# Kernel tuning notes

Hardware: AMD Instinct MI355X
Metric: run time of the kernel (lower is better)

## Reference

```python
import jax, jax.numpy as jnp
import numpy as np

IN_F = 4096
OUT_F = 4096
RANK = 16
ALPHA = 16
SCALING = ALPHA / RANK  # 1.0


def setup_inputs() -> dict:
    key = jax.random.key(0)
    k_x, k_w, k_b, k_a = jax.random.split(key, 4)
    x = jax.random.normal(k_x, (4, 2048, IN_F), dtype=jnp.float32)
    # frozen base linear params
    W = jax.random.normal(k_w, (OUT_F, IN_F), dtype=jnp.float32) * (1.0 / np.sqrt(IN_F))
    b = jax.random.normal(k_b, (OUT_F,), dtype=jnp.float32) * 0.01
    # LoRA params: A kaiming-uniform-like, B zeros per initial_weights(); use small
    bound = np.sqrt(6.0 / IN_F)  # kaiming_uniform(a=sqrt(5)) bound approx
    lora_A = jax.random.uniform(k_a, (RANK, IN_F), dtype=jnp.float32, minval=-bound, maxval=bound)
    lora_B = jax.random.normal(jax.random.fold_in(key, 7), (OUT_F, RANK), dtype=jnp.float32) * 0.01
    lora_bias = jnp.zeros((OUT_F,), dtype=jnp.float32)
    return {"x": x, "W": W, "b": b, "lora_A": lora_A, "lora_B": lora_B, "lora_bias": lora_bias}


def reference(x, W, b, lora_A, lora_B, lora_bias):
    # Original: F.linear(x, W + scaling*B@A, bias=b + lora_bias); dropout is Identity (p=0).
    # Algebraically equivalent form avoiding the [out,in] delta materialization:
    # y = x@W^T + scaling * (x@A^T)@B^T + (b + lora_bias)
    base = jnp.einsum('bsi,oi->bso', x, W)
    low = jnp.einsum('bsr,or->bso', jnp.einsum('bsi,ri->bsr', x, lora_A), lora_B)
    return base + SCALING * low + (b + lora_bias)
```

## Files before the change

### kernel.cpp

```cpp
#include <hip/hip_runtime.h>
#include <hip/hip_bf16.h>
#include <stdint.h>


#define M_DIM 8192
#define N_DIM 4096
#define K_DIM 4096
#define NT    (K_DIM / 64)

typedef __attribute__((ext_vector_type(8))) short bf16x8;
typedef __attribute__((ext_vector_type(4))) float f32x4;

#define BARRIER() __builtin_amdgcn_s_barrier()
#define WAITV8() asm volatile("s_waitcnt vmcnt(8)" ::: "memory")
#define WAITV0() asm volatile("s_waitcnt vmcnt(0)" ::: "memory")

static __device__ __forceinline__ unsigned short f2bf(float f) {
    unsigned int u = __builtin_bit_cast(unsigned int, f);
    unsigned int r = (u + 0x7fffu + ((u >> 16) & 1u)) >> 16;
    return (unsigned short)r;
}

__global__ __launch_bounds__(256) void conv_x_kernel(
    const float* __restrict__ x, unsigned short* __restrict__ xb) {
    size_t i = ((size_t)blockIdx.x * 256 + threadIdx.x) * 8;
    float4 a = *(const float4*)(x + i);
    float4 c = *(const float4*)(x + i + 4);
    union { unsigned short us[8]; uint4 v; } u;
    u.us[0] = f2bf(a.x); u.us[1] = f2bf(a.y); u.us[2] = f2bf(a.z); u.us[3] = f2bf(a.w);
    u.us[4] = f2bf(c.x); u.us[5] = f2bf(c.y); u.us[6] = f2bf(c.z); u.us[7] = f2bf(c.w);
    *(uint4*)(xb + i) = u.v;
}

__global__ __launch_bounds__(512) void conv_w_kernel(
    const float* __restrict__ W, const float* __restrict__ lA,
    const float* __restrict__ lB, unsigned short* __restrict__ Wb) {
    const int nb = blockIdx.x * 4;
    const int k0 = threadIdx.x * 8;

    float acc[4][8];
#pragma unroll
    for (int r = 0; r < 4; ++r) {
        const float4* w4 = (const float4*)(W + (size_t)(nb + r) * K_DIM + k0);
        float4 v0 = w4[0], v1 = w4[1];
        acc[r][0] = v0.x; acc[r][1] = v0.y; acc[r][2] = v0.z; acc[r][3] = v0.w;
        acc[r][4] = v1.x; acc[r][5] = v1.y; acc[r][6] = v1.z; acc[r][7] = v1.w;
    }
    float brs[4][16];
#pragma unroll
    for (int r = 0; r < 4; ++r)
#pragma unroll
        for (int t = 0; t < 16; ++t) brs[r][t] = lB[(size_t)(nb + r) * 16 + t];

#pragma unroll
    for (int t = 0; t < 16; ++t) {
        const float4* a4 = (const float4*)(lA + (size_t)t * K_DIM + k0);
        float4 v0 = a4[0], v1 = a4[1];
        float av[8] = {v0.x, v0.y, v0.z, v0.w, v1.x, v1.y, v1.z, v1.w};
#pragma unroll
        for (int r = 0; r < 4; ++r)
#pragma unroll
            for (int j = 0; j < 8; ++j) acc[r][j] += brs[r][t] * av[j];
    }
#pragma unroll
    for (int r = 0; r < 4; ++r) {
        union { unsigned short us[8]; uint4 v; } u;
#pragma unroll
        for (int j = 0; j < 8; ++j) u.us[j] = f2bf(acc[r][j]);
        *(uint4*)(Wb + (size_t)(nb + r) * K_DIM + k0) = u.v;
    }
}

__global__ __launch_bounds__(512, 2) void gemm_kernel(
    const unsigned short* __restrict__ A,
    const unsigned short* __restrict__ B,
    const float* __restrict__ bvec, const float* __restrict__ lbvec,
    float* __restrict__ C) {
    const int tid = threadIdx.x;
    const int lane = tid & 63;
    const int wid = tid >> 6;
    const int wr = wid >> 2;
    const int wc = wid & 3;

    const int bid = blockIdx.x;
    const int ntile = (bid & 7) * 2 + ((bid >> 3) & 1);
    const int mtile = bid >> 4;
    const int m0 = mtile * 256, n0 = ntile * 256;

    __shared__ __align__(16) unsigned short ldsA[2 * 2 * 128 * 64];
    __shared__ __align__(16) unsigned short ldsB[2 * 2 * 128 * 64];

    const int lr8 = lane >> 3;
    const int cch = (lane & 7) ^ lr8;
    const unsigned short* aSb = A + (size_t)(m0 + lr8) * K_DIM + cch * 8;
    const unsigned short* bSb = B + (size_t)(n0 + lr8) * K_DIM + cch * 8;

    auto stageA = [&](int par_, int h, int kt) {
#pragma unroll
        for (int s = 0; s < 2; ++s) {
            const int j = wid * 2 + s;
            const unsigned short* g = aSb + (size_t)(h * 128 + j * 8) * K_DIM + kt * 64;
            __builtin_amdgcn_global_load_lds(
                (const __attribute__((address_space(1))) void*)g,
                (__attribute__((address_space(3))) void*)(ldsA + (par_ * 2 + h) * 8192 + j * 512),
                16, 0, 0);
        }
    };
    auto stageB = [&](int par_, int h, int kt) {
#pragma unroll
        for (int s = 0; s < 2; ++s) {
            const int j = wid * 2 + s;
            const unsigned short* g = bSb + (size_t)(h * 128 + j * 8) * K_DIM + kt * 64;
            __builtin_amdgcn_global_load_lds(
                (const __attribute__((address_space(1))) void*)g,
                (__attribute__((address_space(3))) void*)(ldsB + (par_ * 2 + h) * 8192 + j * 512),
                16, 0, 0);
        }
    };

    const int rowByte = (lane & 15) * 128;
    const int swz = (lane & 7) << 4;
    const int kc0 = (0 * 64 + (lane >> 4) * 16) ^ swz;
    const int kc1 = (1 * 64 + (lane >> 4) * 16) ^ swz;
    const int baseBoff = (wc & 1) * 4096;

    auto readA = [&](int par_, int mf, int kk) -> bf16x8 {
        const char* p = (const char*)(ldsA + (par_ * 2 + wr) * 8192 + mf * 1024) +
                        rowByte + (kk ? kc1 : kc0);
        return *(const bf16x8*)p;
    };
    auto readB = [&](int par_, int nf, int kk) -> bf16x8 {
        const char* p = (const char*)(ldsB + (par_ * 2 + (wc >> 1)) * 8192 + baseBoff + nf * 1024) +
                        rowByte + (kk ? kc1 : kc0);
        return *(const bf16x8*)p;
    };

    f32x4 acc[8][4] = {};
    bf16x8 A_[4], B0_[4], B1_[4];

    stageB(0, 0, 0); stageB(0, 1, 0); stageA(0, 0, 0); stageA(0, 1, 0);
    stageB(1, 0, 1); stageB(1, 1, 1); stageA(1, 0, 1); stageA(1, 1, 1);
    WAITV8();
    BARRIER();

#define KTILE(kt, par)                                                          \
    {                                                                           \
        _Pragma("unroll") for (int i = 0; i < 4; ++i) A_[i] = readA(par, i, 0); \
        _Pragma("unroll") for (int j = 0; j < 4; ++j) B0_[j] = readB(par, j, 0);\
        _Pragma("unroll") for (int j = 0; j < 4; ++j) B1_[j] = readB(par, j, 1);\
        __builtin_amdgcn_s_setprio(1);                                          \
        _Pragma("unroll") for (int i = 0; i < 4; ++i)                           \
            _Pragma("unroll") for (int j = 0; j < 4; ++j)                       \
                acc[i][j] = __builtin_amdgcn_mfma_f32_16x16x32_bf16(            \
                    A_[i], B0_[j], acc[i][j], 0, 0, 0);                         \
        __builtin_amdgcn_s_setprio(0);                                          \
        _Pragma("unroll") for (int i = 0; i < 4; ++i) A_[i] = readA(par, 4 + i, 0); \
        __builtin_amdgcn_s_setprio(1);                                          \
        _Pragma("unroll") for (int i = 0; i < 4; ++i)                           \
            _Pragma("unroll") for (int j = 0; j < 4; ++j)                       \
                acc[4 + i][j] = __builtin_amdgcn_mfma_f32_16x16x32_bf16(        \
                    A_[i], B0_[j], acc[4 + i][j], 0, 0, 0);                     \
        __builtin_amdgcn_s_setprio(0);                                          \
        _Pragma("unroll") for (int i = 0; i < 4; ++i) A_[i] = readA(par, i, 1); \
        __builtin_amdgcn_s_setprio(1);                                          \
        _Pragma("unroll") for (int i = 0; i < 4; ++i)                           \
            _Pragma("unroll") for (int j = 0; j < 4; ++j)                       \
                acc[i][j] = __builtin_amdgcn_mfma_f32_16x16x32_bf16(            \
                    A_[i], B1_[j], acc[i][j], 0, 0, 0);                         \
        __builtin_amdgcn_s_setprio(0);                                          \
        _Pragma("unroll") for (int i = 0; i < 4; ++i) A_[i] = readA(par, 4 + i, 1); \
        __builtin_amdgcn_s_setprio(1);                                          \
        _Pragma("unroll") for (int i = 0; i < 4; ++i)                           \
            _Pragma("unroll") for (int j = 0; j < 4; ++j)                       \
                acc[4 + i][j] = __builtin_amdgcn_mfma_f32_16x16x32_bf16(        \
                    A_[i], B1_[j], acc[4 + i][j], 0, 0, 0);                     \
        __builtin_amdgcn_s_setprio(0);                                          \
        BARRIER();                                                              \
        if ((kt) + 2 < NT) {                                                    \
            stageB(par, 0, (kt) + 2); stageB(par, 1, (kt) + 2);                 \
            stageA(par, 0, (kt) + 2); stageA(par, 1, (kt) + 2);                 \
            WAITV8();                                                           \
        } else { WAITV0(); }                                                    \
        BARRIER();                                                              \
    }

#pragma unroll 1
    for (int kt = 0; kt < NT; kt += 2) {
        KTILE(kt, 0);
        KTILE(kt + 1, 1);
    }
#undef KTILE

#pragma unroll
    for (int nf = 0; nf < 4; ++nf) {
        const int gc = n0 + wc * 64 + nf * 16 + (lane & 15);
        const float bv = bvec[gc] + lbvec[gc];
#pragma unroll
        for (int mf = 0; mf < 8; ++mf) {
            const int gr0 = m0 + wr * 128 + mf * 16 + (lane >> 4) * 4;
            f32x4 v = acc[mf][nf];
#pragma unroll
            for (int j = 0; j < 4; ++j)
                __builtin_nontemporal_store(v[j] + bv, &C[(size_t)(gr0 + j) * N_DIM + gc]);
        }
    }
}

__global__ __launch_bounds__(256) void naive_kernel(
    const float* __restrict__ x, const float* __restrict__ W,
    const float* __restrict__ b, const float* __restrict__ lA,
    const float* __restrict__ lB, const float* __restrict__ lb,
    float* __restrict__ out) {
    __shared__ float xs[K_DIM];
    __shared__ float ts[16];
    const int m = blockIdx.x;
    const int tid = threadIdx.x;
    for (int k = tid; k < K_DIM; k += 256) xs[k] = x[(size_t)m * K_DIM + k];
    if (tid < 16) ts[tid] = 0.f;
    __syncthreads();
    float part[16] = {};
    for (int k = tid * 16; k < tid * 16 + 16; ++k) {
        float xv = xs[k];
#pragma unroll
        for (int r = 0; r < 16; ++r) part[r] += xv * lA[(size_t)r * K_DIM + k];
    }
#pragma unroll
    for (int r = 0; r < 16; ++r) atomicAdd(&ts[r], part[r]);
    __syncthreads();
    const int n = blockIdx.y * 256 + tid;
    float acc = b[n] + lb[n];
#pragma unroll
    for (int r = 0; r < 16; ++r) acc += ts[r] * lB[(size_t)n * 16 + r];
    const float* wrow = W + (size_t)n * K_DIM;
    for (int k = 0; k < K_DIM; ++k) acc += xs[k] * wrow[k];
    out[(size_t)m * N_DIM + n] = acc;
}

extern "C" void kernel_launch(void* const* d_in, const int* in_sizes, int n_in,
                              void* d_out, int out_size, void* d_ws, size_t ws_size,
                              hipStream_t stream) {
    const float* x  = (const float*)d_in[0];
    const float* W  = (const float*)d_in[1];
    const float* b  = (const float*)d_in[2];
    const float* lA = (const float*)d_in[3];
    const float* lB = (const float*)d_in[4];
    const float* lb = (const float*)d_in[5];
    float* out = (float*)d_out;

    const size_t xb_bytes = (size_t)M_DIM * K_DIM * 2;
    const size_t wb_bytes = (size_t)N_DIM * K_DIM * 2;

    if (ws_size >= xb_bytes + wb_bytes) {
        unsigned short* xb = (unsigned short*)d_ws;
        unsigned short* wb = (unsigned short*)((char*)d_ws + xb_bytes);

        conv_x_kernel<<<(M_DIM * K_DIM) / (256 * 8), 256, 0, stream>>>(x, xb);
        conv_w_kernel<<<N_DIM / 4, 512, 0, stream>>>(W, lA, lB, wb);

        gemm_kernel<<<(M_DIM / 256) * (N_DIM / 256), 512, 0, stream>>>(xb, wb, b, lb, out);
    } else {
        dim3 grid(M_DIM, N_DIM / 256);
        naive_kernel<<<grid, 256, 0, stream>>>(x, W, b, lA, lB, lb, out);
    }
}
```

Measured before the change: 330.2 us.

## Switch GEMM inner loop to 32x32x16 MFMA with software-pipelined LDS reads

```diff
diff --git a/kernel.cpp b/kernel.cpp
--- a/kernel.cpp
+++ b/kernel.cpp
@@ -8,12 +8,14 @@
 #define K_DIM 4096
 #define NT    (K_DIM / 64)
 
-typedef __attribute__((ext_vector_type(8))) short bf16x8;
-typedef __attribute__((ext_vector_type(4))) float f32x4;
+typedef __attribute__((ext_vector_type(8)))  short bf16x8;
+typedef __attribute__((ext_vector_type(16))) float f32x16;
 
 #define BARRIER() __builtin_amdgcn_s_barrier()
 #define WAITV8() asm volatile("s_waitcnt vmcnt(8)" ::: "memory")
 #define WAITV0() asm volatile("s_waitcnt vmcnt(0)" ::: "memory")
+#define LGKMC(n) asm volatile("s_waitcnt lgkmcnt(" #n ")" ::: "memory")
+#define SCHED_FENCE() __builtin_amdgcn_sched_barrier(0)
 
 static __device__ __forceinline__ unsigned short f2bf(float f) {
     unsigned int u = __builtin_bit_cast(unsigned int, f);
@@ -117,91 +119,97 @@
                 16, 0, 0);
         }
     };
-
-    const int rowByte = (lane & 15) * 128;
+    auto stageTile = [&](int par_, int kt) {
+        stageB(par_, 0, kt); stageB(par_, 1, kt);
+        stageA(par_, 0, kt); stageA(par_, 1, kt);
+    };
+
+    const int rowA = (lane & 31);
     const int swz = (lane & 7) << 4;
-    const int kc0 = (0 * 64 + (lane >> 4) * 16) ^ swz;
-    const int kc1 = (1 * 64 + (lane >> 4) * 16) ^ swz;
-    const int baseBoff = (wc & 1) * 4096;
-
-    auto readA = [&](int par_, int mf, int kk) -> bf16x8 {
-        const char* p = (const char*)(ldsA + (par_ * 2 + wr) * 8192 + mf * 1024) +
-                        rowByte + (kk ? kc1 : kc0);
+    const int kbase = (lane >> 5) * 16;
+
+    auto readA32 = [&](int par_, int mf, int ks) -> bf16x8 {
+        const int row = mf * 32 + rowA;
+        const char* p = (const char*)(ldsA + (par_ * 2 + wr) * 8192) +
+                        row * 128 + ((ks * 32 + kbase) ^ swz);
         return *(const bf16x8*)p;
     };
-    auto readB = [&](int par_, int nf, int kk) -> bf16x8 {
-        const char* p = (const char*)(ldsB + (par_ * 2 + (wc >> 1)) * 8192 + baseBoff + nf * 1024) +
-                        rowByte + (kk ? kc1 : kc0);
+    auto readB32 = [&](int par_, int nf, int ks) -> bf16x8 {
+        const int row = (wc & 1) * 64 + nf * 32 + rowA;
+        const char* p = (const char*)(ldsB + (par_ * 2 + (wc >> 1)) * 8192) +
+                        row * 128 + ((ks * 32 + kbase) ^ swz);
         return *(const bf16x8*)p;
     };
 
-    f32x4 acc[8][4] = {};
-    bf16x8 A_[4], B0_[4], B1_[4];
-
-    stageB(0, 0, 0); stageB(0, 1, 0); stageA(0, 0, 0); stageA(0, 1, 0);
-    stageB(1, 0, 1); stageB(1, 1, 1); stageA(1, 0, 1); stageA(1, 1, 1);
+    f32x16 acc[4][2] = {};
+    bf16x8 sa0[4], sb0[2], sa1[4], sb1[2];
+
+#define READS0(par_, ks) do { \
+    _Pragma("unroll") for (int mf = 0; mf < 4; ++mf) sa0[mf] = readA32(par_, mf, ks); \
+    _Pragma("unroll") for (int nf = 0; nf < 2; ++nf) sb0[nf] = readB32(par_, nf, ks); } while (0)
+#define READS1(par_, ks) do { \
+    _Pragma("unroll") for (int mf = 0; mf < 4; ++mf) sa1[mf] = readA32(par_, mf, ks); \
+    _Pragma("unroll") for (int nf = 0; nf < 2; ++nf) sb1[nf] = readB32(par_, nf, ks); } while (0)
+#define BURST0() do { __builtin_amdgcn_s_setprio(1); \
+    _Pragma("unroll") for (int mf = 0; mf < 4; ++mf) \
+        _Pragma("unroll") for (int nf = 0; nf < 2; ++nf) \
+            acc[mf][nf] = __builtin_amdgcn_mfma_f32_32x32x16_bf16( \
+                sa0[mf], sb0[nf], acc[mf][nf], 0, 0, 0); \
+    __builtin_amdgcn_s_setprio(0); } while (0)
+#define BURST1() do { __builtin_amdgcn_s_setprio(1); \
+    _Pragma("unroll") for (int mf = 0; mf < 4; ++mf) \
+        _Pragma("unroll") for (int nf = 0; nf < 2; ++nf) \
+            acc[mf][nf] = __builtin_amdgcn_mfma_f32_32x32x16_bf16( \
+                sa1[mf], sb1[nf], acc[mf][nf], 0, 0, 0); \
+    __builtin_amdgcn_s_setprio(0); } while (0)
+
+    stageTile(0, 0);
+    stageTile(1, 1);
     WAITV8();
     BARRIER();
 
-#define KTILE(kt, par)                                                          \
-    {                                                                           \
-        _Pragma("unroll") for (int i = 0; i < 4; ++i) A_[i] = readA(par, i, 0); \
-        _Pragma("unroll") for (int j = 0; j < 4; ++j) B0_[j] = readB(par, j, 0);\
-        _Pragma("unroll") for (int j = 0; j < 4; ++j) B1_[j] = readB(par, j, 1);\
-        __builtin_amdgcn_s_setprio(1);                                          \
-        _Pragma("unroll") for (int i = 0; i < 4; ++i)                           \
-            _Pragma("unroll") for (int j = 0; j < 4; ++j)                       \
-                acc[i][j] = __builtin_amdgcn_mfma_f32_16x16x32_bf16(            \
-                    A_[i], B0_[j], acc[i][j], 0, 0, 0);                         \
-        __builtin_amdgcn_s_setprio(0);                                          \
-        _Pragma("unroll") for (int i = 0; i < 4; ++i) A_[i] = readA(par, 4 + i, 0); \
-        __builtin_amdgcn_s_setprio(1);                                          \
-        _Pragma("unroll") for (int i = 0; i < 4; ++i)                           \
-            _Pragma("unroll") for (int j = 0; j < 4; ++j)                       \
-                acc[4 + i][j] = __builtin_amdgcn_mfma_f32_16x16x32_bf16(        \
-                    A_[i], B0_[j], acc[4 + i][j], 0, 0, 0);                     \
-        __builtin_amdgcn_s_setprio(0);                                          \
-        _Pragma("unroll") for (int i = 0; i < 4; ++i) A_[i] = readA(par, i, 1); \
-        __builtin_amdgcn_s_setprio(1);                                          \
-        _Pragma("unroll") for (int i = 0; i < 4; ++i)                           \
-            _Pragma("unroll") for (int j = 0; j < 4; ++j)                       \
-                acc[i][j] = __builtin_amdgcn_mfma_f32_16x16x32_bf16(            \
-                    A_[i], B1_[j], acc[i][j], 0, 0, 0);                         \
-        __builtin_amdgcn_s_setprio(0);                                          \
-        _Pragma("unroll") for (int i = 0; i < 4; ++i) A_[i] = readA(par, 4 + i, 1); \
-        __builtin_amdgcn_s_setprio(1);                                          \
-        _Pragma("unroll") for (int i = 0; i < 4; ++i)                           \
-            _Pragma("unroll") for (int j = 0; j < 4; ++j)                       \
-                acc[4 + i][j] = __builtin_amdgcn_mfma_f32_16x16x32_bf16(        \
-                    A_[i], B1_[j], acc[4 + i][j], 0, 0, 0);                     \
-        __builtin_amdgcn_s_setprio(0);                                          \
-        BARRIER();                                                              \
-        if ((kt) + 2 < NT) {                                                    \
-            stageB(par, 0, (kt) + 2); stageB(par, 1, (kt) + 2);                 \
-            stageA(par, 0, (kt) + 2); stageA(par, 1, (kt) + 2);                 \
-            WAITV8();                                                           \
-        } else { WAITV0(); }                                                    \
-        BARRIER();                                                              \
-    }
-
 #pragma unroll 1
-    for (int kt = 0; kt < NT; kt += 2) {
-        KTILE(kt, 0);
-        KTILE(kt + 1, 1);
-    }
-#undef KTILE
-
-#pragma unroll
-    for (int nf = 0; nf < 4; ++nf) {
-        const int gc = n0 + wc * 64 + nf * 16 + (lane & 15);
+    for (int kt = 0; kt < NT; ++kt) {
+        const int par = kt & 1;
+        READS0(par, 0);
+        READS1(par, 1);
+        SCHED_FENCE();
+        LGKMC(6); SCHED_FENCE();
+        BURST0();
+        READS0(par, 2);
+        SCHED_FENCE();
+        LGKMC(6); SCHED_FENCE();
+        BURST1();
+        READS1(par, 3);
+        SCHED_FENCE();
+        LGKMC(6); SCHED_FENCE();
+        BURST0();
+        LGKMC(0); SCHED_FENCE();
+        BURST1();
+        BARRIER();
+        if (kt + 2 < NT) { stageTile(par, kt + 2); WAITV8(); }
+        else { WAITV0(); }
+        BARRIER();
+    }
+
+#undef READS0
+#undef READS1
+#undef BURST0
+#undef BURST1
+
+#pragma unroll
+    for (int nf = 0; nf < 2; ++nf) {
+        const int gc = n0 + wc * 64 + nf * 32 + (lane & 31);
         const float bv = bvec[gc] + lbvec[gc];
 #pragma unroll
-        for (int mf = 0; mf < 8; ++mf) {
-            const int gr0 = m0 + wr * 128 + mf * 16 + (lane >> 4) * 4;
-            f32x4 v = acc[mf][nf];
-#pragma unroll
-            for (int j = 0; j < 4; ++j)
-                __builtin_nontemporal_store(v[j] + bv, &C[(size_t)(gr0 + j) * N_DIM + gc]);
+        for (int mf = 0; mf < 4; ++mf) {
+            const int gr0 = m0 + wr * 128 + mf * 32 + 4 * (lane >> 5);
+            f32x16 v = acc[mf][nf];
+#pragma unroll
+            for (int r = 0; r < 16; ++r) {
+                const int row = gr0 + (r & 3) + 8 * (r >> 2);
+                __builtin_nontemporal_store(v[r] + bv, &C[(size_t)row * N_DIM + gc]);
+            }
         }
     }
 }
```

New measurement: 332.6 us. Within noise of the previous version (+0.7%).
